# Optimization experiments

Measured on AMD Instinct MI355X. Metric: run time of the kernel, lower is better.

Reference implementation:

```python
import jax, jax.numpy as jnp
from jax import lax
import numpy as np

IN, H1, H2 = 16, 64, 1


def _init_lstm(key, in_dim, hid):
    k = 1.0 / np.sqrt(hid)
    k1, k2, k3, k4 = jax.random.split(key, 4)
    u = lambda kk, shp: jax.random.uniform(kk, shp, jnp.float32, -k, k)
    return u(k1, (4 * hid, in_dim)), u(k2, (4 * hid, hid)), u(k3, (4 * hid,)), u(k4, (4 * hid,))


def setup_inputs() -> dict:
    key = jax.random.key(0)
    kx, k1, k2, kf = jax.random.split(key, 4)
    x = jax.random.normal(kx, (4096, 256, IN), jnp.float32)
    w_ih1, w_hh1, b_ih1, b_hh1 = _init_lstm(k1, IN, H1)
    w_ih2, w_hh2, b_ih2, b_hh2 = _init_lstm(k2, H1, H2)
    kfw, kfb = jax.random.split(kf)
    fc_w = jax.random.uniform(kfw, (1, 1), jnp.float32, -1.0, 1.0)
    fc_b = jax.random.uniform(kfb, (1,), jnp.float32, -1.0, 1.0)
    return {"x": x,
            "w_ih1": w_ih1, "w_hh1": w_hh1, "b_ih1": b_ih1, "b_hh1": b_hh1,
            "w_ih2": w_ih2, "w_hh2": w_hh2, "b_ih2": b_ih2, "b_hh2": b_hh2,
            "fc_w": fc_w, "fc_b": fc_b}


def _lstm(x, w_ih, w_hh, b_ih, b_hh):
    # x: [B, T, in]; PyTorch gate order: i, f, g, o
    B = x.shape[0]
    H = w_hh.shape[1]
    # precompute input projection for all timesteps (big GEMM outside recurrence)
    xg = jnp.einsum('bti,gi->btg', x, w_ih) + b_ih + b_hh  # [B, T, 4H]

    def step(carry, xg_t):
        h, c = carry
        gates = xg_t + h @ w_hh.T  # [B, 4H]
        i, f, g, o = jnp.split(gates, 4, axis=-1)
        i = jax.nn.sigmoid(i)
        f = jax.nn.sigmoid(f)
        g = jnp.tanh(g)
        o = jax.nn.sigmoid(o)
        c = f * c + i * g
        h = o * jnp.tanh(c)
        return (h, c), h

    h0 = jnp.zeros((B, H), x.dtype)
    (_, _), hs = lax.scan(step, (h0, h0), jnp.swapaxes(xg, 0, 1))  # hs: [T, B, H]
    return jnp.swapaxes(hs, 0, 1)  # [B, T, H]


def reference(x, w_ih1, w_hh1, b_ih1, b_hh1, w_ih2, w_hh2, b_ih2, b_hh2, fc_w, fc_b):
    h = _lstm(x, w_ih1, w_hh1, b_ih1, b_hh1)   # [B, T, 64]
    h = _lstm(h, w_ih2, w_hh2, b_ih2, b_hh2)   # [B, T, 1]
    return h @ fc_w.T + fc_b                     # [B, T, 1]
```

## Files before the change

kernel.cpp:

```cpp
#include <hip/hip_runtime.h>

typedef float  f32x4  __attribute__((ext_vector_type(4)));
typedef __bf16 bf16x8 __attribute__((ext_vector_type(8)));
typedef unsigned short u16x4 __attribute__((ext_vector_type(4)));
typedef unsigned short u16x8 __attribute__((ext_vector_type(8)));

#define NL2E (-1.44269504088896f)
#define TL2E ( 2.88539008177793f)

__device__ __forceinline__ float rcpf(float x) { return __builtin_amdgcn_rcpf(x); }
__device__ __forceinline__ float ex2(float x)  { return __builtin_amdgcn_exp2f(x); }

__device__ __forceinline__ float cell_update(float zi, float zf, float zg, float zo, float& c) {
    const float Ei = ex2(zi), Ef = ex2(zf), Eg = ex2(zg), Eo = ex2(zo);
    const float ig = (Eg - 1.0f) * rcpf((1.0f + Ei) * (1.0f + Eg));
    const float fv = rcpf(1.0f + Ef);
    c = __builtin_fmaf(fv, c, ig);
    const float zc = fminf(fmaxf(TL2E * c, -60.0f), 60.0f);
    const float Ec = ex2(zc);
    return (Ec - 1.0f) * rcpf((1.0f + Eo) * (1.0f + Ec));
}

__global__ __launch_bounds__(1024, 1) void lstm_fused(
    const float* __restrict__ x,
    const float* __restrict__ w_ih1,
    const float* __restrict__ w_hh1,
    const float* __restrict__ b_ih1, const float* __restrict__ b_hh1,
    const float* __restrict__ w_ih2,
    const float* __restrict__ w_hh2,
    const float* __restrict__ b_ih2, const float* __restrict__ b_hh2,
    const float* __restrict__ fc_w, const float* __restrict__ fc_b,
    float* __restrict__ out)
{
    __shared__ unsigned short A_h[2 * 16 * 64];
    __shared__ unsigned short Xc[2 * 16 * 16 * 32];
    __shared__ float Pre2[2][64];
    __shared__ float Ybuf[16][16];

    const int tid = threadIdx.x;
    const int w   = tid >> 6;
    const int l   = tid & 63;
    const int q   = l & 15;
    const int hi  = l >> 4;
    const int b0  = blockIdx.x << 4;
    const int sw  = (q & 7) << 4;
    const u16x8 z8 = {0,0,0,0,0,0,0,0};

    if (tid < 256) ((u16x8*)A_h)[tid] = z8;
    {
        const int buf = tid >> 9, zb = (tid >> 5) & 15, ztt = (tid >> 1) & 15, zh = tid & 1;
        *(u16x8*)((char*)Xc + buf * 16384 + zb * 1024
                  + ((ztt * 64 + 32 + zh * 16) ^ ((zb & 7) << 4))) = z8;
    }

    const int gq = q >> 2;
    const int gate_col = (gq << 6) + (w << 2) + (q & 3);
    const float sc = (gq == 2) ? TL2E : NL2E;
    bf16x8 Bf[3];
    #pragma unroll
    for (int ks = 0; ks < 3; ++ks) {
        bf16x8 tmp;
        #pragma unroll
        for (int j = 0; j < 8; ++j) {
            const int k = ks * 32 + hi * 8 + j;
            float v = 0.f;
            if (k < 64)      v = w_hh1[gate_col * 64 + k];
            else if (k < 80) v = w_ih1[gate_col * 16 + (k - 64)];
            tmp[j] = (__bf16)(sc * v);
        }
        Bf[ks] = tmp;
    }
    bf16x8 B2[2];
    {
        const float sc2 = (q == 2) ? TL2E : NL2E;
        #pragma unroll
        for (int ks = 0; ks < 2; ++ks) {
            bf16x8 tmp;
            #pragma unroll
            for (int j = 0; j < 8; ++j) {
                const int k = ks * 32 + hi * 8 + j;
                const float v = (q < 4) ? w_ih2[q * 64 + k] : 0.f;
                tmp[j] = (__bf16)(sc2 * v);
            }
            B2[ks] = tmp;
        }
    }
    const float accb = sc * (b_ih1[gate_col] + b_hh1[gate_col]);

    const float w2si = NL2E * w_hh2[0], w2sf = NL2E * w_hh2[1];
    const float w2sg = TL2E * w_hh2[2], w2so = NL2E * w_hh2[3];
    const float nb2i = NL2E * (b_ih2[0] + b_hh2[0]);
    const float nb2f = NL2E * (b_ih2[1] + b_hh2[1]);
    const float tb2g = TL2E * (b_ih2[2] + b_hh2[2]);
    const float nb2o = NL2E * (b_ih2[3] + b_hh2[3]);
    const float fcw = fc_w[0], fcb = fc_b[0];

    const int bx = tid >> 6, part = (tid >> 2) & 15, qu = tid & 3;
    const unsigned xoff = (unsigned)(bx * 1024 + ((part * 64 + qu * 8) ^ ((bx & 7) << 4)));
    const float* xrow = x + (size_t)(b0 + bx) * 4096 + part * 16 + qu * 4;
    f32x4 xq;
    auto stage_x = [&](int bufoff) {
        u16x4 v;
        #pragma unroll
        for (int j = 0; j < 4; ++j) v[j] = __builtin_bit_cast(unsigned short, (__bf16)xq[j]);
        *(u16x4*)((char*)Xc + bufoff + xoff) = v;
    };
    xq = *(const f32x4*)xrow;
    stage_x(0);
    xq = *(const f32x4*)(xrow + 256);

    const unsigned ar0 = (unsigned)((q * 128 +      hi * 16) ^ sw);
    const unsigned ar1 = (unsigned)((q * 128 + 64 + hi * 16) ^ sw);
    const int bb = (hi << 2) + gq;
    const int he = (w << 2) + (q & 3);
    const unsigned awh = (unsigned)(bb * 128 + ((he * 2) ^ ((bb & 7) << 4)));

    float cc = 0.f, h2 = 0.f, c2 = 0.f;
    __syncthreads();

    #pragma unroll 2
    for (int t = 0; t < 256; ++t) {
        const int tt = t & 15;
        if (tt == 0 && t + 16 < 256) {
            stage_x(((((t >> 4) + 1) & 1)) << 14);
            if (t + 32 < 256) xq = *(const f32x4*)(xrow + (t + 32) * 16);
        }

        const int rb = ((t + 1) & 1) << 11;
        const u16x8 ra0 = *(const u16x8*)((const char*)A_h + rb + ar0);
        const u16x8 ra1 = *(const u16x8*)((const char*)A_h + rb + ar1);
        const u16x8 ra2 = *(const u16x8*)((const char*)Xc + (((t >> 4) & 1) << 14)
                                          + ((q * 1024 + (tt << 6) + (hi << 4)) ^ sw));
        f32x4 p2;
        if (w == 14 && l < 16) p2 = *(const f32x4*)&Pre2[(t + 1) & 1][l << 2];

        const bf16x8 a0 = __builtin_bit_cast(bf16x8, ra0);
        const bf16x8 a1 = __builtin_bit_cast(bf16x8, ra1);
        const bf16x8 a2 = __builtin_bit_cast(bf16x8, ra2);

        f32x4 g = {accb, accb, accb, accb};
        g = __builtin_amdgcn_mfma_f32_16x16x32_bf16(a2, Bf[2], g, 0, 0, 0);
        g = __builtin_amdgcn_mfma_f32_16x16x32_bf16(a0, Bf[0], g, 0, 0, 0);
        g = __builtin_amdgcn_mfma_f32_16x16x32_bf16(a1, Bf[1], g, 0, 0, 0);

        if (w == 15) {
            f32x4 p4 = {0.f, 0.f, 0.f, 0.f};
            p4 = __builtin_amdgcn_mfma_f32_16x16x32_bf16(a0, B2[0], p4, 0, 0, 0);
            p4 = __builtin_amdgcn_mfma_f32_16x16x32_bf16(a1, B2[1], p4, 0, 0, 0);
            if (q < 4) {
                #pragma unroll
                for (int r = 0; r < 4; ++r) Pre2[t & 1][((hi << 2) + r) * 4 + q] = p4[r];
            }
        }
        if (w == 14 && t >= 2) {
            const int s = t - 2;
            if (l < 16) {
                const float zi = p2[0] + __builtin_fmaf(w2si, h2, nb2i);
                const float zf = p2[1] + __builtin_fmaf(w2sf, h2, nb2f);
                const float zg = p2[2] + __builtin_fmaf(w2sg, h2, tb2g);
                const float zo = p2[3] + __builtin_fmaf(w2so, h2, nb2o);
                h2 = cell_update(zi, zf, zg, zo, c2);
                Ybuf[l][s & 15] = __builtin_fmaf(fcw, h2, fcb);
            }
            if ((s & 15) == 15) {
                float* op = out + (size_t)(b0 + (l >> 2)) * 256 + (s - 15) + ((l & 3) << 2);
                *(f32x4*)op = *(const f32x4*)&Ybuf[l >> 2][(l & 3) << 2];
            }
        }

        float v0 = g[0], v1 = g[1], v2 = g[2], v3 = g[3];
        {
            const bool od = (q & 4);
            float x0 = od ? v0 : v1;
            float x1 = od ? v2 : v3;
            const float y0 = __shfl_xor(x0, 4, 64);
            const float y1 = __shfl_xor(x1, 4, 64);
            if (od) { v0 = y0; v2 = y1; } else { v1 = y0; v3 = y1; }
        }
        {
            const bool od = (q & 8);
            float x0 = od ? v0 : v2;
            float x1 = od ? v1 : v3;
            const float y0 = __shfl_xor(x0, 8, 64);
            const float y1 = __shfl_xor(x1, 8, 64);
            if (od) { v0 = y0; v1 = y1; } else { v2 = y0; v3 = y1; }
        }
        const float hv = cell_update(v0, v1, v2, v3, cc);
        *(unsigned short*)((char*)A_h + ((t & 1) << 11) + awh) =
            __builtin_bit_cast(unsigned short, (__bf16)hv);

        __syncthreads();
    }

    if (w == 15) {
        const u16x8 ra0 = *(const u16x8*)((const char*)A_h + 2048 + ar0);
        const u16x8 ra1 = *(const u16x8*)((const char*)A_h + 2048 + ar1);
        f32x4 p4 = {0.f, 0.f, 0.f, 0.f};
        p4 = __builtin_amdgcn_mfma_f32_16x16x32_bf16(__builtin_bit_cast(bf16x8, ra0), B2[0], p4, 0, 0, 0);
        p4 = __builtin_amdgcn_mfma_f32_16x16x32_bf16(__builtin_bit_cast(bf16x8, ra1), B2[1], p4, 0, 0, 0);
        if (q < 4) {
            #pragma unroll
            for (int r = 0; r < 4; ++r) Pre2[0][((hi << 2) + r) * 4 + q] = p4[r];
        }
    }
    __syncthreads();
    if (w == 14) {
        if (l < 16) {
            #pragma unroll
            for (int e = 0; e < 2; ++e) {
                const f32x4 p2 = *(const f32x4*)&Pre2[1 - e][l << 2];
                const float zi = p2[0] + __builtin_fmaf(w2si, h2, nb2i);
                const float zf = p2[1] + __builtin_fmaf(w2sf, h2, nb2f);
                const float zg = p2[2] + __builtin_fmaf(w2sg, h2, tb2g);
                const float zo = p2[3] + __builtin_fmaf(w2so, h2, nb2o);
                h2 = cell_update(zi, zf, zg, zo, c2);
                Ybuf[l][14 + e] = __builtin_fmaf(fcw, h2, fcb);
            }
        }
        float* op = out + (size_t)(b0 + (l >> 2)) * 256 + 240 + ((l & 3) << 2);
        *(f32x4*)op = *(const f32x4*)&Ybuf[l >> 2][(l & 3) << 2];
    }
}

extern "C" void kernel_launch(void* const* d_in, const int* in_sizes, int n_in,
                              void* d_out, int out_size, void* d_ws, size_t ws_size,
                              hipStream_t stream) {
    (void)in_sizes; (void)n_in; (void)out_size; (void)d_ws; (void)ws_size;
    const float* x     = (const float*)d_in[0];
    const float* w_ih1 = (const float*)d_in[1];
    const float* w_hh1 = (const float*)d_in[2];
    const float* b_ih1 = (const float*)d_in[3];
    const float* b_hh1 = (const float*)d_in[4];
    const float* w_ih2 = (const float*)d_in[5];
    const float* w_hh2 = (const float*)d_in[6];
    const float* b_ih2 = (const float*)d_in[7];
    const float* b_hh2 = (const float*)d_in[8];
    const float* fc_w  = (const float*)d_in[9];
    const float* fc_b  = (const float*)d_in[10];
    lstm_fused<<<dim3(256), dim3(1024), 0, stream>>>(
        x, w_ih1, w_hh1, b_ih1, b_hh1, w_ih2, w_hh2, b_ih2, b_hh2, fc_w, fc_b,
        (float*)d_out);
}
```

Baseline: 193.6 us.

## Halve block to 8 waves, each computing two gate tiles per step

The block shrinks from 16 to 8 wavefronts. Each wave now owns 8 hidden units and issues two MFMA accumulation chains (T0/T1), so the gate exchange needs one shuffle stage instead of two, and each lane updates two LSTM cells per step. The x staging loads 8 floats per thread to match the smaller block. The aim is to cut per-step barrier cost and wave count in the latency-bound recurrence, at the price of more serial work per wave on the critical path.

New measurement: 167.4 us. 1.16x faster.

```diff
diff --git a/kernel.cpp b/kernel.cpp
--- a/kernel.cpp
+++ b/kernel.cpp
@@ -2,7 +2,6 @@
 
 typedef float  f32x4  __attribute__((ext_vector_type(4)));
 typedef __bf16 bf16x8 __attribute__((ext_vector_type(8)));
-typedef unsigned short u16x4 __attribute__((ext_vector_type(4)));
 typedef unsigned short u16x8 __attribute__((ext_vector_type(8)));
 
 #define NL2E (-1.44269504088896f)
@@ -21,7 +20,7 @@
     return (Ec - 1.0f) * rcpf((1.0f + Eo) * (1.0f + Ec));
 }
 
-__global__ __launch_bounds__(1024, 1) void lstm_fused(
+__global__ __launch_bounds__(512, 1) void lstm_fused(
     const float* __restrict__ x,
     const float* __restrict__ w_ih1,
     const float* __restrict__ w_hh1,
@@ -42,33 +41,41 @@
     const int l   = tid & 63;
     const int q   = l & 15;
     const int hi  = l >> 4;
+    const int qh  = q >> 3;
     const int b0  = blockIdx.x << 4;
     const int sw  = (q & 7) << 4;
     const u16x8 z8 = {0,0,0,0,0,0,0,0};
 
     if (tid < 256) ((u16x8*)A_h)[tid] = z8;
     {
-        const int buf = tid >> 9, zb = (tid >> 5) & 15, ztt = (tid >> 1) & 15, zh = tid & 1;
-        *(u16x8*)((char*)Xc + buf * 16384 + zb * 1024
-                  + ((ztt * 64 + 32 + zh * 16) ^ ((zb & 7) << 4))) = z8;
-    }
-
-    const int gq = q >> 2;
-    const int gate_col = (gq << 6) + (w << 2) + (q & 3);
-    const float sc = (gq == 2) ? TL2E : NL2E;
-    bf16x8 Bf[3];
+        const int buf = tid >> 8, zb = (tid >> 4) & 15, ztt = tid & 15;
+        char* zp = (char*)Xc + buf * 16384 + zb * 1024;
+        *(u16x8*)(zp + ((ztt * 64 + 32) ^ ((zb & 7) << 4))) = z8;
+        *(u16x8*)(zp + ((ztt * 64 + 48) ^ ((zb & 7) << 4))) = z8;
+    }
+
+    const int hb8 = w << 3;
+    bf16x8 Bf[2][3];
+    float accb[2];
     #pragma unroll
-    for (int ks = 0; ks < 3; ++ks) {
-        bf16x8 tmp;
+    for (int tile = 0; tile < 2; ++tile) {
+        const int gate = (tile << 1) + qh;
+        const int gcol = (gate << 6) + hb8 + (q & 7);
+        const float sc = (gate == 2) ? TL2E : NL2E;
         #pragma unroll
-        for (int j = 0; j < 8; ++j) {
-            const int k = ks * 32 + hi * 8 + j;
-            float v = 0.f;
-            if (k < 64)      v = w_hh1[gate_col * 64 + k];
-            else if (k < 80) v = w_ih1[gate_col * 16 + (k - 64)];
-            tmp[j] = (__bf16)(sc * v);
-        }
-        Bf[ks] = tmp;
+        for (int ks = 0; ks < 3; ++ks) {
+            bf16x8 tmp;
+            #pragma unroll
+            for (int j = 0; j < 8; ++j) {
+                const int k = ks * 32 + hi * 8 + j;
+                float v = 0.f;
+                if (k < 64)      v = w_hh1[gcol * 64 + k];
+                else if (k < 80) v = w_ih1[gcol * 16 + (k - 64)];
+                tmp[j] = (__bf16)(sc * v);
+            }
+            Bf[tile][ks] = tmp;
+        }
+        accb[tile] = sc * (b_ih1[gcol] + b_hh1[gcol]);
     }
     bf16x8 B2[2];
     {
@@ -85,7 +92,6 @@
             B2[ks] = tmp;
         }
     }
-    const float accb = sc * (b_ih1[gate_col] + b_hh1[gate_col]);
 
     const float w2si = NL2E * w_hh2[0], w2sf = NL2E * w_hh2[1];
     const float w2sg = TL2E * w_hh2[2], w2so = NL2E * w_hh2[3];
@@ -95,27 +101,33 @@
     const float nb2o = NL2E * (b_ih2[3] + b_hh2[3]);
     const float fcw = fc_w[0], fcb = fc_b[0];
 
-    const int bx = tid >> 6, part = (tid >> 2) & 15, qu = tid & 3;
-    const unsigned xoff = (unsigned)(bx * 1024 + ((part * 64 + qu * 8) ^ ((bx & 7) << 4)));
-    const float* xrow = x + (size_t)(b0 + bx) * 4096 + part * 16 + qu * 4;
-    f32x4 xq;
+    const int bx = tid >> 5, rem = tid & 31, part = rem >> 1, half = rem & 1;
+    const unsigned xoff = (unsigned)(bx * 1024 + ((part * 64 + half * 16) ^ ((bx & 7) << 4)));
+    const float* xrow = x + (size_t)(b0 + bx) * 4096 + part * 16 + half * 8;
+    f32x4 xqa, xqb;
+    auto ldx = [&](int t) {
+        const float* p = xrow + t * 16;
+        xqa = ((const f32x4*)p)[0]; xqb = ((const f32x4*)p)[1];
+    };
     auto stage_x = [&](int bufoff) {
-        u16x4 v;
+        bf16x8 v;
         #pragma unroll
-        for (int j = 0; j < 4; ++j) v[j] = __builtin_bit_cast(unsigned short, (__bf16)xq[j]);
-        *(u16x4*)((char*)Xc + bufoff + xoff) = v;
+        for (int j = 0; j < 4; ++j) { v[j] = (__bf16)xqa[j]; v[4 + j] = (__bf16)xqb[j]; }
+        *(u16x8*)((char*)Xc + bufoff + xoff) = __builtin_bit_cast(u16x8, v);
     };
-    xq = *(const f32x4*)xrow;
-    stage_x(0);
-    xq = *(const f32x4*)(xrow + 256);
+    ldx(0); stage_x(0); ldx(16);
 
     const unsigned ar0 = (unsigned)((q * 128 +      hi * 16) ^ sw);
     const unsigned ar1 = (unsigned)((q * 128 + 64 + hi * 16) ^ sw);
-    const int bb = (hi << 2) + gq;
-    const int he = (w << 2) + (q & 3);
-    const unsigned awh = (unsigned)(bb * 128 + ((he * 2) ^ ((bb & 7) << 4)));
-
-    float cc = 0.f, h2 = 0.f, c2 = 0.f;
+    const int he = hb8 + (q & 7);
+    const int bA = (hi << 2) + (qh << 1);
+    const int bB = bA + 1;
+    const unsigned awA = (unsigned)(bA * 128 + ((he * 2) ^ ((bA & 7) << 4)));
+    const unsigned awB = (unsigned)(bB * 128 + ((he * 2) ^ ((bB & 7) << 4)));
+
+    float cA = 0.f, cB = 0.f;
+    float h2 = 0.f, c2 = 0.f;
+
     __syncthreads();
 
     #pragma unroll 2
@@ -123,7 +135,7 @@
         const int tt = t & 15;
         if (tt == 0 && t + 16 < 256) {
             stage_x(((((t >> 4) + 1) & 1)) << 14);
-            if (t + 32 < 256) xq = *(const f32x4*)(xrow + (t + 32) * 16);
+            if (t + 32 < 256) ldx(t + 32);
         }
 
         const int rb = ((t + 1) & 1) << 11;
@@ -131,19 +143,21 @@
         const u16x8 ra1 = *(const u16x8*)((const char*)A_h + rb + ar1);
         const u16x8 ra2 = *(const u16x8*)((const char*)Xc + (((t >> 4) & 1) << 14)
                                           + ((q * 1024 + (tt << 6) + (hi << 4)) ^ sw));
-        f32x4 p2;
-        if (w == 14 && l < 16) p2 = *(const f32x4*)&Pre2[(t + 1) & 1][l << 2];
 
         const bf16x8 a0 = __builtin_bit_cast(bf16x8, ra0);
         const bf16x8 a1 = __builtin_bit_cast(bf16x8, ra1);
         const bf16x8 a2 = __builtin_bit_cast(bf16x8, ra2);
 
-        f32x4 g = {accb, accb, accb, accb};
-        g = __builtin_amdgcn_mfma_f32_16x16x32_bf16(a2, Bf[2], g, 0, 0, 0);
-        g = __builtin_amdgcn_mfma_f32_16x16x32_bf16(a0, Bf[0], g, 0, 0, 0);
-        g = __builtin_amdgcn_mfma_f32_16x16x32_bf16(a1, Bf[1], g, 0, 0, 0);
-
-        if (w == 15) {
+        f32x4 T0 = {accb[0], accb[0], accb[0], accb[0]};
+        f32x4 T1 = {accb[1], accb[1], accb[1], accb[1]};
+        T0 = __builtin_amdgcn_mfma_f32_16x16x32_bf16(a2, Bf[0][2], T0, 0, 0, 0);
+        T1 = __builtin_amdgcn_mfma_f32_16x16x32_bf16(a2, Bf[1][2], T1, 0, 0, 0);
+        T0 = __builtin_amdgcn_mfma_f32_16x16x32_bf16(a0, Bf[0][0], T0, 0, 0, 0);
+        T1 = __builtin_amdgcn_mfma_f32_16x16x32_bf16(a0, Bf[1][0], T1, 0, 0, 0);
+        T0 = __builtin_amdgcn_mfma_f32_16x16x32_bf16(a1, Bf[0][1], T0, 0, 0, 0);
+        T1 = __builtin_amdgcn_mfma_f32_16x16x32_bf16(a1, Bf[1][1], T1, 0, 0, 0);
+
+        if (w == 7) {
             f32x4 p4 = {0.f, 0.f, 0.f, 0.f};
             p4 = __builtin_amdgcn_mfma_f32_16x16x32_bf16(a0, B2[0], p4, 0, 0, 0);
             p4 = __builtin_amdgcn_mfma_f32_16x16x32_bf16(a1, B2[1], p4, 0, 0, 0);
@@ -152,9 +166,10 @@
                 for (int r = 0; r < 4; ++r) Pre2[t & 1][((hi << 2) + r) * 4 + q] = p4[r];
             }
         }
-        if (w == 14 && t >= 2) {
+        if (w == 6 && t >= 2) {
             const int s = t - 2;
             if (l < 16) {
+                const f32x4 p2 = *(const f32x4*)&Pre2[(t + 1) & 1][l << 2];
                 const float zi = p2[0] + __builtin_fmaf(w2si, h2, nb2i);
                 const float zf = p2[1] + __builtin_fmaf(w2sf, h2, nb2f);
                 const float zg = p2[2] + __builtin_fmaf(w2sg, h2, tb2g);
@@ -168,31 +183,30 @@
             }
         }
 
-        float v0 = g[0], v1 = g[1], v2 = g[2], v3 = g[3];
-        {
-            const bool od = (q & 4);
-            float x0 = od ? v0 : v1;
-            float x1 = od ? v2 : v3;
-            const float y0 = __shfl_xor(x0, 4, 64);
-            const float y1 = __shfl_xor(x1, 4, 64);
-            if (od) { v0 = y0; v2 = y1; } else { v1 = y0; v3 = y1; }
-        }
-        {
-            const bool od = (q & 8);
-            float x0 = od ? v0 : v2;
-            float x1 = od ? v1 : v3;
-            const float y0 = __shfl_xor(x0, 8, 64);
-            const float y1 = __shfl_xor(x1, 8, 64);
-            if (od) { v0 = y0; v1 = y1; } else { v2 = y0; v3 = y1; }
-        }
-        const float hv = cell_update(v0, v1, v2, v3, cc);
-        *(unsigned short*)((char*)A_h + ((t & 1) << 11) + awh) =
-            __builtin_bit_cast(unsigned short, (__bf16)hv);
+        const bool lo = (qh == 0);
+        const float s1 = lo ? T0[2] : T0[0];
+        const float s2 = lo ? T0[3] : T0[1];
+        const float s3 = lo ? T1[2] : T1[0];
+        const float s4 = lo ? T1[3] : T1[1];
+        const float r1 = __shfl_xor(s1, 8, 64);
+        const float r2 = __shfl_xor(s2, 8, 64);
+        const float r3 = __shfl_xor(s3, 8, 64);
+        const float r4 = __shfl_xor(s4, 8, 64);
+        const float ziA = lo ? T0[0] : r1,  ziB = lo ? T0[1] : r2;
+        const float zfA = lo ? r1 : T0[2],  zfB = lo ? r2 : T0[3];
+        const float zgA = lo ? T1[0] : r3,  zgB = lo ? T1[1] : r4;
+        const float zoA = lo ? r3 : T1[2],  zoB = lo ? r4 : T1[3];
+
+        char* AW = (char*)A_h + ((t & 1) << 11);
+        const float hvA = cell_update(ziA, zfA, zgA, zoA, cA);
+        *(unsigned short*)(AW + awA) = __builtin_bit_cast(unsigned short, (__bf16)hvA);
+        const float hvB = cell_update(ziB, zfB, zgB, zoB, cB);
+        *(unsigned short*)(AW + awB) = __builtin_bit_cast(unsigned short, (__bf16)hvB);
 
         __syncthreads();
     }
 
-    if (w == 15) {
+    if (w == 7) {
         const u16x8 ra0 = *(const u16x8*)((const char*)A_h + 2048 + ar0);
         const u16x8 ra1 = *(const u16x8*)((const char*)A_h + 2048 + ar1);
         f32x4 p4 = {0.f, 0.f, 0.f, 0.f};
@@ -204,7 +218,7 @@
         }
     }
     __syncthreads();
-    if (w == 14) {
+    if (w == 6) {
         if (l < 16) {
             #pragma unroll
             for (int e = 0; e < 2; ++e) {
@@ -237,7 +251,7 @@
     const float* b_hh2 = (const float*)d_in[8];
     const float* fc_w  = (const float*)d_in[9];
     const float* fc_b  = (const float*)d_in[10];
-    lstm_fused<<<dim3(256), dim3(1024), 0, stream>>>(
+    lstm_fused<<<dim3(256), dim3(512), 0, stream>>>(
         x, w_ih1, w_hh1, b_ih1, b_hh1, w_ih2, w_hh2, b_ih2, b_hh2, fc_w, fc_b,
         (float*)d_out);
 }
```
